# Kernel tuning notes

Measured on AMD Instinct MI355X. Metric: run time of the kernel, lower is better.

Reference implementation:

```python
import jax, jax.numpy as jnp
import numpy as np


def setup_inputs() -> dict:
    key = jax.random.key(0)
    k1, k2 = jax.random.split(key)
    n_tokens, embed_dim, num_embed = 16384, 512, 2048
    encode = jax.random.normal(k1, (n_tokens, embed_dim), dtype=jnp.float32)
    # Embedding init in torch: uniform(-1/num_embed, 1/num_embed)
    templat = jax.random.uniform(
        k2, (num_embed, embed_dim), dtype=jnp.float32,
        minval=-1.0 / num_embed, maxval=1.0 / num_embed)
    return {"encode": encode, "templat": templat}


def reference(encode, templat):
    # match_encode_with_templat, eval path: sample=False, detach='encode', metric='l2'
    encode_d = jax.lax.stop_gradient(encode)
    # squared L2 distance: ||e||^2 - 2 e@t^T + ||t||^2 ; logits = -dist
    e_sq = jnp.sum(encode_d * encode_d, axis=-1, keepdims=True)       # (N, 1)
    t_sq = jnp.sum(templat * templat, axis=-1)[None, :]               # (1, M)
    dist = e_sq - 2.0 * (encode_d @ templat.T) + t_sq                 # (N, M)
    logits = -dist
    zsoft = jax.nn.softmax(logits, axis=-1)
    zidx = jnp.argmax(zsoft, axis=-1)                                 # (N,)
    quant = templat[zidx]                                             # (N, C) gather
    return quant, zidx
```

## Files before the change

kernel.cpp:

```cpp
#include <hip/hip_runtime.h>
#include <stdint.h>

#define N_TOK  16384
#define EMB    512
#define NEMB   2048
#define NCHUNK 32
#define CWIN   2.5e-4f
#define WCAP   524288

typedef __attribute__((ext_vector_type(8))) short s16x8;
typedef __attribute__((ext_vector_type(4))) float f32x4;

__device__ __forceinline__ unsigned short f2bf(float f) {
  unsigned u = __float_as_uint(f);
  u += 0x7fffu + ((u >> 16) & 1u);
  return (unsigned short)(u >> 16);
}
__device__ __forceinline__ unsigned mapf(float f) {
  unsigned u = __float_as_uint(f);
  return (u >> 31) ? ~u : (u | 0x80000000u);
}
__device__ __forceinline__ float unmapf(unsigned u) {
  return __uint_as_float((u >> 31) ? (u & 0x7fffffffu) : ~u);
}

__device__ __forceinline__ float pairwise512_sq(const float* se, int lane) {
  int l = lane & 31;
  int b = l >> 3, j = l & 7;
  const float* base = se + b * 128 + j;
  float x = base[0];
  float r = __fmul_rn(x, x);
#pragma unroll
  for (int k = 1; k < 16; ++k) {
    float y = base[8 * k];
    r = __fadd_rn(r, __fmul_rn(y, y));
  }
  r = __fadd_rn(r, __shfl_xor(r, 1));
  r = __fadd_rn(r, __shfl_xor(r, 2));
  r = __fadd_rn(r, __shfl_xor(r, 4));
  r = __fadd_rn(r, __shfl_xor(r, 8));
  r = __fadd_rn(r, __shfl_xor(r, 16));
  return r;
}

__global__ __launch_bounds__(256) void prep_kernel(
    const float* __restrict__ tmp, const float* __restrict__ enc,
    unsigned short* __restrict__ thi, float* __restrict__ tsq,
    unsigned short* __restrict__ ehi, float* __restrict__ esq,
    int* __restrict__ wcount) {
  __shared__ float se[4][EMB];
  int wv = threadIdx.x >> 6, lane = threadIdx.x & 63;
  int row = blockIdx.x * 4 + wv;
  if (blockIdx.x == 0 && threadIdx.x == 0) *wcount = 0;
  bool isT = row < NEMB;
  const float* src = isT ? (tmp + (size_t)row * EMB)
                         : (enc + (size_t)(row - NEMB) * EMB);
  const float4* p = (const float4*)src + lane * 2;
  float4 v0 = p[0], v1 = p[1];
  float f[8] = {v0.x, v0.y, v0.z, v0.w, v1.x, v1.y, v1.z, v1.w};
  unsigned h[8];
#pragma unroll
  for (int i = 0; i < 8; ++i) { h[i] = f2bf(f[i]); se[wv][lane * 8 + i] = f[i]; }
  uint4 packed = { h[0] | (h[1] << 16), h[2] | (h[3] << 16),
                   h[4] | (h[5] << 16), h[6] | (h[7] << 16) };
  unsigned short* dsth = isT ? (thi + (size_t)row * EMB)
                             : (ehi + (size_t)(row - NEMB) * EMB);
  ((uint4*)dsth)[lane] = packed;
  __syncthreads();
  float s = pairwise512_sq(se[wv], lane);
  if (lane == 0) { if (isT) tsq[row] = s; else esq[row - NEMB] = s; }
}

__global__ __launch_bounds__(512, 2) void score_kernel(
    const unsigned short* __restrict__ ehi, const unsigned short* __restrict__ thi,
    const float* __restrict__ tsq,
    unsigned long long* __restrict__ keyc, unsigned* __restrict__ s2c) {
  __shared__ __align__(16) char smem[131072];
  const int tid = threadIdx.x, w = tid >> 6, lane = tid & 63;
  const int q = lane >> 4, r = lane & 15;
  const int wr = w >> 2, wc = w & 3;
  const int tokb = (int)blockIdx.x >> 3;
  const int nb   = (int)blockIdx.x & 7;

  const int c0 = tid, c1 = 512 + tid;
  const int L0 = (c0 * 16) ^ ((((c0 * 16) >> 9) & 1) << 5);
  const int L1 = (c1 * 16) ^ ((((c1 * 16) >> 9) & 1) << 5);
  const int row0 = L0 >> 6, ce0 = (L0 & 63) >> 1;
  const int row1 = L1 >> 6, ce1 = (L1 & 63) >> 1;
  const unsigned short* pa0 = ehi + (size_t)(tokb * 256 + row0) * EMB + ce0;
  const unsigned short* pa1 = ehi + (size_t)(tokb * 256 + row1) * EMB + ce1;
  const unsigned short* pb0 = thi + (size_t)(nb  * 256 + row0) * EMB + ce0;
  const unsigned short* pb1 = thi + (size_t)(nb  * 256 + row1) * EMB + ce1;

#define STAGE_A(ktp, kk) do {                                                     \
    char* lb_ = smem + ((((ktp) & 1) * 2 + (kk)) << 14) + (w << 10);              \
    __builtin_amdgcn_global_load_lds(                                             \
        (const __attribute__((address_space(1))) void*)(pa0 + (ktp) * 64 + (kk) * 32), \
        (__attribute__((address_space(3))) void*)lb_, 16, 0, 0);                  \
    __builtin_amdgcn_global_load_lds(                                             \
        (const __attribute__((address_space(1))) void*)(pa1 + (ktp) * 64 + (kk) * 32), \
        (__attribute__((address_space(3))) void*)(lb_ + 8192), 16, 0, 0);         \
  } while (0)
#define STAGE_B(ktp, kk) do {                                                     \
    char* lb_ = smem + 65536 + ((((ktp) & 1) * 2 + (kk)) << 14) + (w << 10);      \
    __builtin_amdgcn_global_load_lds(                                             \
        (const __attribute__((address_space(1))) void*)(pb0 + (ktp) * 64 + (kk) * 32), \
        (__attribute__((address_space(3))) void*)lb_, 16, 0, 0);                  \
    __builtin_amdgcn_global_load_lds(                                             \
        (const __attribute__((address_space(1))) void*)(pb1 + (ktp) * 64 + (kk) * 32), \
        (__attribute__((address_space(3))) void*)(lb_ + 8192), 16, 0, 0);         \
  } while (0)

  int offA[8], offB[4];
#pragma unroll
  for (int m = 0; m < 8; ++m) {
    int P = (wr * 128 + m * 16 + r) * 64 + q * 16;
    offA[m] = P ^ (((P >> 9) & 1) << 5);
  }
#pragma unroll
  for (int n = 0; n < 4; ++n) {
    int P = (wc * 64 + n * 16 + r) * 64 + q * 16;
    offB[n] = P ^ (((P >> 9) & 1) << 5);
  }

  f32x4 acc[8][4];
#pragma unroll
  for (int m = 0; m < 8; ++m)
#pragma unroll
    for (int n = 0; n < 4; ++n) acc[m][n] = (f32x4){0.f, 0.f, 0.f, 0.f};

  STAGE_A(0, 0); STAGE_B(0, 0); STAGE_A(0, 1); STAGE_B(0, 1); STAGE_A(1, 0); STAGE_B(1, 0);
  asm volatile("s_waitcnt vmcnt(8)" ::: "memory");
  __builtin_amdgcn_s_barrier();

#define LOADA(kkbase, mh)                                        \
    a0 = *(const s16x8*)(Ab_ + (kkbase) + offA[(mh) * 4 + 0]);   \
    a1 = *(const s16x8*)(Ab_ + (kkbase) + offA[(mh) * 4 + 1]);   \
    a2 = *(const s16x8*)(Ab_ + (kkbase) + offA[(mh) * 4 + 2]);   \
    a3 = *(const s16x8*)(Ab_ + (kkbase) + offA[(mh) * 4 + 3]);
#define LOADB(kkbase)                                            \
    bf4[0] = *(const s16x8*)(Bb_ + (kkbase) + offB[0]);          \
    bf4[1] = *(const s16x8*)(Bb_ + (kkbase) + offB[1]);          \
    bf4[2] = *(const s16x8*)(Bb_ + (kkbase) + offB[2]);          \
    bf4[3] = *(const s16x8*)(Bb_ + (kkbase) + offB[3]);
#define MFMA_HALF(mh)                                                              \
    __builtin_amdgcn_s_setprio(1);                                                 \
    _Pragma("unroll")                                                              \
    for (int n = 0; n < 4; ++n) {                                                  \
      acc[(mh) * 4 + 0][n] = __builtin_amdgcn_mfma_f32_16x16x32_bf16(a0, bf4[n], acc[(mh) * 4 + 0][n], 0, 0, 0); \
      acc[(mh) * 4 + 1][n] = __builtin_amdgcn_mfma_f32_16x16x32_bf16(a1, bf4[n], acc[(mh) * 4 + 1][n], 0, 0, 0); \
      acc[(mh) * 4 + 2][n] = __builtin_amdgcn_mfma_f32_16x16x32_bf16(a2, bf4[n], acc[(mh) * 4 + 2][n], 0, 0, 0); \
      acc[(mh) * 4 + 3][n] = __builtin_amdgcn_mfma_f32_16x16x32_bf16(a3, bf4[n], acc[(mh) * 4 + 3][n], 0, 0, 0); \
    }                                                                              \
    __builtin_amdgcn_s_setprio(0);

#pragma unroll
  for (int kt = 0; kt < 8; ++kt) {
    char* Ab_ = smem + ((kt & 1) * 2 << 14);
    char* Bb_ = smem + 65536 + ((kt & 1) * 2 << 14);
    s16x8 a0, a1, a2, a3, bf4[4];
    LOADA(0, 0); LOADB(0);
    if (kt + 1 < 8) STAGE_A(kt + 1, 1);
    __builtin_amdgcn_s_barrier();
    MFMA_HALF(0);
    __builtin_amdgcn_s_barrier();
    LOADA(0, 1);
    if (kt + 1 < 8) STAGE_B(kt + 1, 1);
    __builtin_amdgcn_s_barrier();
    MFMA_HALF(1);
    if (kt < 7) { asm volatile("s_waitcnt vmcnt(8)" ::: "memory"); }
    else        { asm volatile("s_waitcnt vmcnt(0)" ::: "memory"); }
    __builtin_amdgcn_s_barrier();
    LOADA(16384, 0); LOADB(16384);
    if (kt + 2 < 8) STAGE_A(kt + 2, 0);
    __builtin_amdgcn_s_barrier();
    MFMA_HALF(0);
    __builtin_amdgcn_s_barrier();
    LOADA(16384, 1);
    if (kt + 2 < 8) STAGE_B(kt + 2, 0);
    __builtin_amdgcn_s_barrier();
    MFMA_HALF(1);
    if (kt < 6)       { asm volatile("s_waitcnt vmcnt(8)" ::: "memory"); }
    else if (kt == 6) { asm volatile("s_waitcnt vmcnt(4)" ::: "memory"); }
    __builtin_amdgcn_s_barrier();
  }

  const int chunk = nb * 4 + wc;
  const int nbase = nb * 256 + wc * 64;
  float tq[4];
#pragma unroll
  for (int n = 0; n < 4; ++n) tq[n] = tsq[nbase + n * 16 + r];
#pragma unroll
  for (int m = 0; m < 8; ++m) {
#pragma unroll
    for (int i = 0; i < 4; ++i) {
      unsigned long long k1 = ~0ULL; unsigned s2m = 0xffffffffu;
#pragma unroll
      for (int n = 0; n < 4; ++n) {
        float s = tq[n] - 2.0f * acc[m][n][i];
        unsigned sm = mapf(s);
        unsigned long long k =
            ((unsigned long long)sm << 32) | (unsigned)(nbase + n * 16 + r);
        if (k < k1) { unsigned o = (unsigned)(k1 >> 32); s2m = o < s2m ? o : s2m; k1 = k; }
        else s2m = sm < s2m ? sm : s2m;
      }
#pragma unroll
      for (int mask = 1; mask < 16; mask <<= 1) {
        unsigned long long ok = __shfl_xor(k1, mask);
        unsigned os = __shfl_xor(s2m, mask);
        if (ok < k1) { unsigned o = (unsigned)(k1 >> 32); s2m = o < s2m ? o : s2m; k1 = ok; }
        else { unsigned o = (unsigned)(ok >> 32); s2m = o < s2m ? o : s2m; }
        s2m = os < s2m ? os : s2m;
      }
      if (r == 0) {
        int token = tokb * 256 + wr * 128 + m * 16 + q * 4 + i;
        keyc[(size_t)chunk * N_TOK + token] = k1;
        s2c [(size_t)chunk * N_TOK + token] = s2m;
      }
    }
  }
#undef STAGE_A
#undef STAGE_B
#undef LOADA
#undef LOADB
#undef MFMA_HALF
}

__global__ __launch_bounds__(256) void merge_kernel(
    const unsigned long long* __restrict__ keyc, const unsigned* __restrict__ s2c,
    int* __restrict__ bestIdx, int* __restrict__ flag, int* __restrict__ work,
    int* __restrict__ wcount, unsigned long long* __restrict__ rkey) {
  int t = blockIdx.x * 256 + threadIdx.x;
  if (t >= N_TOK) return;
  rkey[t] = ~0ULL;
  unsigned long long K = ~0ULL; unsigned S = 0xffffffffu;
  for (int c = 0; c < NCHUNK; ++c) {
    unsigned long long k = keyc[(size_t)c * N_TOK + t];
    unsigned s2 = s2c[(size_t)c * N_TOK + t];
    if (k < K) { unsigned o = (unsigned)(K >> 32); S = o < S ? o : S; K = k; }
    else { unsigned o = (unsigned)(k >> 32); S = o < S ? o : S; }
    S = s2 < S ? s2 : S;
  }
  float best_f   = unmapf((unsigned)(K >> 32));
  float second_f = unmapf(S);
  int idx = (int)(unsigned)(K & 0xffffffffu);
  bestIdx[t] = idx;
  bool ok = (second_f - best_f >= CWIN) && (idx >= 0) && (idx < NEMB) && (best_f == best_f);
  flag[t] = ok ? 0 : 1;
  if (!ok) {
    bool nanCase = !(best_f == best_f);
    float limit = best_f + CWIN;
    for (int c = 0; c < NCHUNK; ++c) {
      float cf = unmapf((unsigned)(keyc[(size_t)c * N_TOK + t] >> 32));
      if (nanCase || !(cf > limit)) {
        int pos = atomicAdd(wcount, 1);
        if (pos < WCAP) work[pos] = t * NCHUNK + c;
      }
    }
  }
}

__global__ __launch_bounds__(256) void refine_kernel(
    const float* __restrict__ enc, const float* __restrict__ tmp,
    const float* __restrict__ esq, const float* __restrict__ tsq,
    const int* __restrict__ work, const int* __restrict__ wcount,
    unsigned long long* __restrict__ rkey) {
  int total = *wcount; if (total > WCAP) total = WCAP;
  __shared__ float se[EMB];
  const int wv = threadIdx.x >> 6, lane = threadIdx.x & 63;
  const int g = lane >> 4, l16 = lane & 15;
  for (int p = blockIdx.x; p < total; p += gridDim.x) {
    __syncthreads();
    int item = work[p];
    int token = item / NCHUNK, c = item % NCHUNK;
    const float4* erow = (const float4*)(enc + (size_t)token * EMB);
    for (int i = threadIdx.x; i < 128; i += 256) ((float4*)se)[i] = erow[i];
    __syncthreads();
    float e2 = esq[token];
    unsigned long long lkey = ~0ULL;
#pragma unroll
    for (int j = 0; j < 4; ++j) {
      int m = c * 64 + wv * 16 + j * 4 + g;
      const float4* trow = (const float4*)(tmp + (size_t)m * EMB);
      double s = 0.0;
#pragma unroll
      for (int k = 0; k < 8; ++k) {
        float4 a = trow[l16 + 16 * k];
        float4 b = ((const float4*)se)[l16 + 16 * k];
        s += (double)a.x * b.x + (double)a.y * b.y
           + (double)a.z * b.z + (double)a.w * b.w;
      }
      s += __shfl_xor(s, 1); s += __shfl_xor(s, 2);
      s += __shfl_xor(s, 4); s += __shfl_xor(s, 8);
      if (l16 == 0) {
        float M  = (float)s;
        float d1 = __fadd_rn(e2, -__fmul_rn(2.0f, M));
        float d2 = __fadd_rn(d1, tsq[m]);
        unsigned long long key =
            ((unsigned long long)__float_as_uint(d2) << 32) | (unsigned)m;
        if (key < lkey) lkey = key;
      }
    }
    if (l16 == 0 && lkey != ~0ULL) atomicMin(&rkey[token], lkey);
  }
}

__global__ void gather_kernel(const float* __restrict__ tmp, const int* __restrict__ bestIdx,
                              const int* __restrict__ flag,
                              const unsigned long long* __restrict__ rkey,
                              float* __restrict__ out) {
  int token = blockIdx.x * 4 + (threadIdx.x >> 6);
  int lane = threadIdx.x & 63;
  int idx = flag[token] ? (int)(unsigned)(rkey[token] & 0xffffffffULL) : bestIdx[token];
  idx = idx < 0 ? 0 : (idx > NEMB - 1 ? NEMB - 1 : idx);
  const float4* src = (const float4*)(tmp + (size_t)idx * EMB) + lane * 2;
  float4* dst = (float4*)(out + (size_t)token * EMB) + lane * 2;
  dst[0] = src[0];
  dst[1] = src[1];
  if (lane == 0) out[(size_t)N_TOK * EMB + token] = (float)idx;
}

extern "C" void kernel_launch(void* const* d_in, const int* in_sizes, int n_in,
                              void* d_out, int out_size, void* d_ws, size_t ws_size,
                              hipStream_t stream) {
  const float* enc = (const float*)d_in[0];
  const float* tmp = (const float*)d_in[1];
  float* out = (float*)d_out;
  char* ws = (char*)d_ws;
  unsigned short* thi = (unsigned short*)ws;
  unsigned short* ehi = (unsigned short*)(ws + 2097152);
  float* tsq      = (float*)(ws + 18874368);
  float* esq      = (float*)(ws + 18882560);
  unsigned long long* keyc = (unsigned long long*)(ws + 18948096);
  unsigned* s2c   = (unsigned*)(ws + 23142400);
  int*   bestIdx  = (int*)  (ws + 25239552);
  int*   flag     = (int*)  (ws + 25305088);
  unsigned long long* rkey = (unsigned long long*)(ws + 25370624);
  int*   wcount   = (int*)  (ws + 25501696);
  int*   work     = (int*)  (ws + 25501760);

  prep_kernel  <<<4608,      256, 0, stream>>>(tmp, enc, thi, tsq, ehi, esq, wcount);
  score_kernel <<<512,       512, 0, stream>>>(ehi, thi, tsq, keyc, s2c);
  merge_kernel <<<N_TOK/256, 256, 0, stream>>>(keyc, s2c, bestIdx, flag, work, wcount, rkey);
  refine_kernel<<<1024,      256, 0, stream>>>(enc, tmp, esq, tsq, work, wcount, rkey);
  gather_kernel<<<N_TOK/4,   256, 0, stream>>>(tmp, bestIdx, flag, rkey, out);
}
```

Measured before the change: 196.1 us.

## Shrink score GEMM tile to 128x128 with triple-buffered K=32 pipeline

Replaces the 256x256 block tile (512 threads, two K-halves, double-buffered 128KB LDS) with a 128x128 tile over 256 threads, a 3-stage ring of K=32 slices in 48KB LDS, and one barrier per step. Launches 2048 blocks instead of 512 to raise occupancy and even out the load across CUs, and uses a new LDS swizzle. The cost is roughly double the global/L2 traffic per FLOP from the smaller tile, and a less overlapped schedule within each block.

```diff
diff --git a/kernel.cpp b/kernel.cpp
--- a/kernel.cpp
+++ b/kernel.cpp
@@ -71,127 +71,96 @@
   if (lane == 0) { if (isT) tsq[row] = s; else esq[row - NEMB] = s; }
 }
 
-__global__ __launch_bounds__(512, 2) void score_kernel(
+__global__ __launch_bounds__(256, 3) void score_kernel(
     const unsigned short* __restrict__ ehi, const unsigned short* __restrict__ thi,
     const float* __restrict__ tsq,
     unsigned long long* __restrict__ keyc, unsigned* __restrict__ s2c) {
-  __shared__ __align__(16) char smem[131072];
+  __shared__ __align__(16) char smem[49152];
   const int tid = threadIdx.x, w = tid >> 6, lane = tid & 63;
   const int q = lane >> 4, r = lane & 15;
-  const int wr = w >> 2, wc = w & 3;
-  const int tokb = (int)blockIdx.x >> 3;
-  const int nb   = (int)blockIdx.x & 7;
-
-  const int c0 = tid, c1 = 512 + tid;
-  const int L0 = (c0 * 16) ^ ((((c0 * 16) >> 9) & 1) << 5);
-  const int L1 = (c1 * 16) ^ ((((c1 * 16) >> 9) & 1) << 5);
-  const int row0 = L0 >> 6, ce0 = (L0 & 63) >> 1;
-  const int row1 = L1 >> 6, ce1 = (L1 & 63) >> 1;
-  const unsigned short* pa0 = ehi + (size_t)(tokb * 256 + row0) * EMB + ce0;
-  const unsigned short* pa1 = ehi + (size_t)(tokb * 256 + row1) * EMB + ce1;
-  const unsigned short* pb0 = thi + (size_t)(nb  * 256 + row0) * EMB + ce0;
-  const unsigned short* pb1 = thi + (size_t)(nb  * 256 + row1) * EMB + ce1;
-
-#define STAGE_A(ktp, kk) do {                                                     \
-    char* lb_ = smem + ((((ktp) & 1) * 2 + (kk)) << 14) + (w << 10);              \
-    __builtin_amdgcn_global_load_lds(                                             \
-        (const __attribute__((address_space(1))) void*)(pa0 + (ktp) * 64 + (kk) * 32), \
-        (__attribute__((address_space(3))) void*)lb_, 16, 0, 0);                  \
-    __builtin_amdgcn_global_load_lds(                                             \
-        (const __attribute__((address_space(1))) void*)(pa1 + (ktp) * 64 + (kk) * 32), \
-        (__attribute__((address_space(3))) void*)(lb_ + 8192), 16, 0, 0);         \
+  const int wr = w >> 1, wc = w & 1;
+  const int tokb = (int)blockIdx.x >> 4;
+  const int nb   = (int)blockIdx.x & 15;
+
+  const int Lp0 = w * 2048 + lane * 16;
+  const int Lp1 = Lp0 + 1024;
+  const int P0 = Lp0 ^ (((Lp0 >> 7) & 3) << 4);
+  const int P1 = Lp1 ^ (((Lp1 >> 7) & 3) << 4);
+  const int rw0 = P0 >> 6, cc0 = (P0 & 63) >> 1;
+  const int rw1 = P1 >> 6, cc1 = (P1 & 63) >> 1;
+  const unsigned short* paA0 = ehi + (size_t)(tokb * 128 + rw0) * EMB + cc0;
+  const unsigned short* paA1 = ehi + (size_t)(tokb * 128 + rw1) * EMB + cc1;
+  const unsigned short* pbB0 = thi + (size_t)(nb * 128 + rw0) * EMB + cc0;
+  const unsigned short* pbB1 = thi + (size_t)(nb * 128 + rw1) * EMB + cc1;
+
+#define GLD(src, dst)                                                    \
+  __builtin_amdgcn_global_load_lds(                                      \
+      (const __attribute__((address_space(1))) void*)(src),              \
+      (__attribute__((address_space(3))) void*)(dst), 16, 0, 0)
+#define STAGE(t) do {                                                    \
+    char* da_ = smem + ((t) % 3) * 8192 + w * 2048;                      \
+    char* db_ = smem + 24576 + ((t) % 3) * 8192 + w * 2048;              \
+    GLD(paA0 + (t) * 32, da_);                                           \
+    GLD(paA1 + (t) * 32, da_ + 1024);                                    \
+    GLD(pbB0 + (t) * 32, db_);                                           \
+    GLD(pbB1 + (t) * 32, db_ + 1024);                                    \
   } while (0)
-#define STAGE_B(ktp, kk) do {                                                     \
-    char* lb_ = smem + 65536 + ((((ktp) & 1) * 2 + (kk)) << 14) + (w << 10);      \
-    __builtin_amdgcn_global_load_lds(                                             \
-        (const __attribute__((address_space(1))) void*)(pb0 + (ktp) * 64 + (kk) * 32), \
-        (__attribute__((address_space(3))) void*)lb_, 16, 0, 0);                  \
-    __builtin_amdgcn_global_load_lds(                                             \
-        (const __attribute__((address_space(1))) void*)(pb1 + (ktp) * 64 + (kk) * 32), \
-        (__attribute__((address_space(3))) void*)(lb_ + 8192), 16, 0, 0);         \
-  } while (0)
-
-  int offA[8], offB[4];
-#pragma unroll
-  for (int m = 0; m < 8; ++m) {
-    int P = (wr * 128 + m * 16 + r) * 64 + q * 16;
-    offA[m] = P ^ (((P >> 9) & 1) << 5);
+
+  int offA[4], offB[4];
+#pragma unroll
+  for (int m = 0; m < 4; ++m) {
+    int row = wr * 64 + m * 16 + r;
+    int P = row * 64 + q * 16;
+    offA[m] = P ^ (((P >> 7) & 3) << 4);
   }
 #pragma unroll
   for (int n = 0; n < 4; ++n) {
-    int P = (wc * 64 + n * 16 + r) * 64 + q * 16;
-    offB[n] = P ^ (((P >> 9) & 1) << 5);
-  }
-
-  f32x4 acc[8][4];
-#pragma unroll
-  for (int m = 0; m < 8; ++m)
+    int row = wc * 64 + n * 16 + r;
+    int P = row * 64 + q * 16;
+    offB[n] = P ^ (((P >> 7) & 3) << 4);
+  }
+
+  f32x4 acc[4][4];
+#pragma unroll
+  for (int m = 0; m < 4; ++m)
 #pragma unroll
     for (int n = 0; n < 4; ++n) acc[m][n] = (f32x4){0.f, 0.f, 0.f, 0.f};
 
-  STAGE_A(0, 0); STAGE_B(0, 0); STAGE_A(0, 1); STAGE_B(0, 1); STAGE_A(1, 0); STAGE_B(1, 0);
-  asm volatile("s_waitcnt vmcnt(8)" ::: "memory");
+  STAGE(0); STAGE(1);
+  asm volatile("s_waitcnt vmcnt(4)" ::: "memory");
   __builtin_amdgcn_s_barrier();
 
-#define LOADA(kkbase, mh)                                        \
-    a0 = *(const s16x8*)(Ab_ + (kkbase) + offA[(mh) * 4 + 0]);   \
-    a1 = *(const s16x8*)(Ab_ + (kkbase) + offA[(mh) * 4 + 1]);   \
-    a2 = *(const s16x8*)(Ab_ + (kkbase) + offA[(mh) * 4 + 2]);   \
-    a3 = *(const s16x8*)(Ab_ + (kkbase) + offA[(mh) * 4 + 3]);
-#define LOADB(kkbase)                                            \
-    bf4[0] = *(const s16x8*)(Bb_ + (kkbase) + offB[0]);          \
-    bf4[1] = *(const s16x8*)(Bb_ + (kkbase) + offB[1]);          \
-    bf4[2] = *(const s16x8*)(Bb_ + (kkbase) + offB[2]);          \
-    bf4[3] = *(const s16x8*)(Bb_ + (kkbase) + offB[3]);
-#define MFMA_HALF(mh)                                                              \
-    __builtin_amdgcn_s_setprio(1);                                                 \
-    _Pragma("unroll")                                                              \
-    for (int n = 0; n < 4; ++n) {                                                  \
-      acc[(mh) * 4 + 0][n] = __builtin_amdgcn_mfma_f32_16x16x32_bf16(a0, bf4[n], acc[(mh) * 4 + 0][n], 0, 0, 0); \
-      acc[(mh) * 4 + 1][n] = __builtin_amdgcn_mfma_f32_16x16x32_bf16(a1, bf4[n], acc[(mh) * 4 + 1][n], 0, 0, 0); \
-      acc[(mh) * 4 + 2][n] = __builtin_amdgcn_mfma_f32_16x16x32_bf16(a2, bf4[n], acc[(mh) * 4 + 2][n], 0, 0, 0); \
-      acc[(mh) * 4 + 3][n] = __builtin_amdgcn_mfma_f32_16x16x32_bf16(a3, bf4[n], acc[(mh) * 4 + 3][n], 0, 0, 0); \
-    }                                                                              \
+#pragma unroll
+  for (int t = 0; t < 16; ++t) {
+    const char* Ab_ = smem + (t % 3) * 8192;
+    const char* Bb_ = smem + 24576 + (t % 3) * 8192;
+    if (t + 2 < 16) STAGE(t + 2);
+    s16x8 af[4], bf[4];
+#pragma unroll
+    for (int m = 0; m < 4; ++m) af[m] = *(const s16x8*)(Ab_ + offA[m]);
+#pragma unroll
+    for (int n = 0; n < 4; ++n) bf[n] = *(const s16x8*)(Bb_ + offB[n]);
+    __builtin_amdgcn_s_setprio(1);
+#pragma unroll
+    for (int n = 0; n < 4; ++n) {
+      acc[0][n] = __builtin_amdgcn_mfma_f32_16x16x32_bf16(af[0], bf[n], acc[0][n], 0, 0, 0);
+      acc[1][n] = __builtin_amdgcn_mfma_f32_16x16x32_bf16(af[1], bf[n], acc[1][n], 0, 0, 0);
+      acc[2][n] = __builtin_amdgcn_mfma_f32_16x16x32_bf16(af[2], bf[n], acc[2][n], 0, 0, 0);
+      acc[3][n] = __builtin_amdgcn_mfma_f32_16x16x32_bf16(af[3], bf[n], acc[3][n], 0, 0, 0);
+    }
     __builtin_amdgcn_s_setprio(0);
-
-#pragma unroll
-  for (int kt = 0; kt < 8; ++kt) {
-    char* Ab_ = smem + ((kt & 1) * 2 << 14);
-    char* Bb_ = smem + 65536 + ((kt & 1) * 2 << 14);
-    s16x8 a0, a1, a2, a3, bf4[4];
-    LOADA(0, 0); LOADB(0);
-    if (kt + 1 < 8) STAGE_A(kt + 1, 1);
-    __builtin_amdgcn_s_barrier();
-    MFMA_HALF(0);
-    __builtin_amdgcn_s_barrier();
-    LOADA(0, 1);
-    if (kt + 1 < 8) STAGE_B(kt + 1, 1);
-    __builtin_amdgcn_s_barrier();
-    MFMA_HALF(1);
-    if (kt < 7) { asm volatile("s_waitcnt vmcnt(8)" ::: "memory"); }
+    if (t < 14) { asm volatile("s_waitcnt vmcnt(4)" ::: "memory"); }
     else        { asm volatile("s_waitcnt vmcnt(0)" ::: "memory"); }
     __builtin_amdgcn_s_barrier();
-    LOADA(16384, 0); LOADB(16384);
-    if (kt + 2 < 8) STAGE_A(kt + 2, 0);
-    __builtin_amdgcn_s_barrier();
-    MFMA_HALF(0);
-    __builtin_amdgcn_s_barrier();
-    LOADA(16384, 1);
-    if (kt + 2 < 8) STAGE_B(kt + 2, 0);
-    __builtin_amdgcn_s_barrier();
-    MFMA_HALF(1);
-    if (kt < 6)       { asm volatile("s_waitcnt vmcnt(8)" ::: "memory"); }
-    else if (kt == 6) { asm volatile("s_waitcnt vmcnt(4)" ::: "memory"); }
-    __builtin_amdgcn_s_barrier();
-  }
-
-  const int chunk = nb * 4 + wc;
-  const int nbase = nb * 256 + wc * 64;
+  }
+
+  const int chunk = nb * 2 + wc;
+  const int nbase = chunk * 64;
   float tq[4];
 #pragma unroll
   for (int n = 0; n < 4; ++n) tq[n] = tsq[nbase + n * 16 + r];
 #pragma unroll
-  for (int m = 0; m < 8; ++m) {
+  for (int m = 0; m < 4; ++m) {
 #pragma unroll
     for (int i = 0; i < 4; ++i) {
       unsigned long long k1 = ~0ULL; unsigned s2m = 0xffffffffu;
@@ -213,17 +182,14 @@
         s2m = os < s2m ? os : s2m;
       }
       if (r == 0) {
-        int token = tokb * 256 + wr * 128 + m * 16 + q * 4 + i;
+        int token = tokb * 128 + wr * 64 + m * 16 + q * 4 + i;
         keyc[(size_t)chunk * N_TOK + token] = k1;
         s2c [(size_t)chunk * N_TOK + token] = s2m;
       }
     }
   }
-#undef STAGE_A
-#undef STAGE_B
-#undef LOADA
-#undef LOADB
-#undef MFMA_HALF
+#undef GLD
+#undef STAGE
 }
 
 __global__ __launch_bounds__(256) void merge_kernel(
@@ -340,7 +306,7 @@
   int*   work     = (int*)  (ws + 25501760);
 
   prep_kernel  <<<4608,      256, 0, stream>>>(tmp, enc, thi, tsq, ehi, esq, wcount);
-  score_kernel <<<512,       512, 0, stream>>>(ehi, thi, tsq, keyc, s2c);
+  score_kernel <<<2048,      256, 0, stream>>>(ehi, thi, tsq, keyc, s2c);
   merge_kernel <<<N_TOK/256, 256, 0, stream>>>(keyc, s2c, bestIdx, flag, work, wcount, rkey);
   refine_kernel<<<1024,      256, 0, stream>>>(enc, tmp, esq, tsq, work, wcount, rkey);
   gather_kernel<<<N_TOK/4,   256, 0, stream>>>(tmp, bestIdx, flag, rkey, out);
```

New measurement: 192.6 us. No clear change (-1.8%).
